# Kernel tuning notes

Measured on AMD Instinct MI355X. Metric: run time of the kernel, lower is better.

The kernel has to match this reference:

```python
import jax, jax.numpy as jnp
import numpy as np

NUM_HEADS = 4
WINDOW_SIZE = 7
DILATION = 1


def local_mask(height, width, window_size, dilation):
    """[N, N] bool mask: True where token i may attend to token j (dilated 2D window)."""
    radius = window_size // 2
    rows = jnp.arange(height)
    cols = jnp.arange(width)
    r = jnp.repeat(rows, width)          # [N] row index of each flattened token
    c = jnp.tile(cols, height)           # [N] col index of each flattened token
    dr = r[:, None] - r[None, :]         # [N, N]
    dc = c[:, None] - c[None, :]
    within = (jnp.abs(dr) <= radius * dilation) & (jnpp_abs(dc) <= radius * dilation) if False else (
        (jnp.abs(dr) <= radius * dilation) & (jnp.abs(dc) <= radius * dilation)
    )
    on_grid = (dr % dilation == 0) & (dc % dilation == 0)
    return within & on_grid


def setup_inputs() -> dict:
    key = jax.random.key(0)
    kq, kk, kv = jax.random.split(key, 3)
    shape = (2, 64, 64, 64)  # (B, C, H, W)
    q = jax.random.normal(kq, shape, dtype=jnp.float32)
    k = jax.random.normal(kk, shape, dtype=jnp.float32)
    v = jax.random.normal(kv, shape, dtype=jnp.float32)
    return {"q": q, "k": k, "v": v}


def reference(q, k, v):
    B, C, H, W = q.shape
    nh = NUM_HEADS
    hd = C // nh
    N = H * W

    def to_seq(x):
        # (B, C, H, W) -> (B, nh, N, hd)
        x = x.reshape(B, nh, hd, H, W)
        return x.transpose(0, 1, 3, 4, 2).reshape(B, nh, N, hd)

    q_seq = to_seq(q)
    k_seq = to_seq(k)
    v_seq = to_seq(v)

    scale = 1.0 / jnp.sqrt(jnp.asarray(hd, dtype=q.dtype))
    scores = jnp.einsum("bhqd,bhkd->bhqk", q_seq, k_seq) * scale  # [B, nh, N, N]

    mask = local_mask(H, W, WINDOW_SIZE, DILATION)  # [N, N] bool
    neg = jnp.finfo(scores.dtype).min
    scores = jnp.where(mask[None, None, :, :], scores, neg)

    attn = jax.nn.softmax(scores, axis=-1)
    out = jnp.einsum("bhqk,bhkd->bhqd", attn, v_seq)  # [B, nh, N, hd]

    # (B, nh, N, hd) -> (B, C, H, W)
    out = out.reshape(B, nh, H, W, hd).transpose(0, 1, 4, 2, 3).reshape(B, C, H, W)
    return out
```

## Files before the change

### kernel.cpp

```cpp
#include <hip/hip_runtime.h>
#include <hip/hip_bf16.h>
#include <math.h>

#define HD  16
#define HW  4096
#define RAD 3

__device__ __forceinline__ float dpp_shl1(float x) {
#if defined(__has_builtin) && __has_builtin(__builtin_amdgcn_update_dpp)
    return __int_as_float(__builtin_amdgcn_update_dpp(
        0, __float_as_int(x), 0x130 , 0xf, 0xf, true));
#else
    int l = (int)(threadIdx.x & 63);
    return __shfl(x, l + 1, 64);
#endif
}
__device__ __forceinline__ float dpp_shr1(float x) {
#if defined(__has_builtin) && __has_builtin(__builtin_amdgcn_update_dpp)
    return __int_as_float(__builtin_amdgcn_update_dpp(
        0, __float_as_int(x), 0x138 , 0xf, 0xf, true));
#else
    int l = (int)(threadIdx.x & 63);
    return __shfl(x, l - 1, 64);
#endif
}

__global__ __launch_bounds__(512, 2)
void local_attn_kernel(const float* __restrict__ q,
                       const float* __restrict__ k,
                       const float* __restrict__ v,
                       float* __restrict__ out) {
    __shared__ __align__(16) float mb[512 * 34];

    const int tid = threadIdx.x;
    const int c   = tid & 63;
    const int w   = tid >> 6;

    const int bid = blockIdx.x;
    const int r0  = (bid & 31) * 2;
    const int h   = (bid >> 5) & 3;
    const int b   = bid >> 7;
    const int base = (b * 4 + h) * (HD * HW);

    const int  rr     = r0 - RAD + w;
    const bool rvalid = ((unsigned)rr < 64u);
    const bool do0    = rvalid && (w <= 6);
    const bool do1    = rvalid && (w >= 1);
    const int  rrc    = rr < 0 ? 0 : (rr > 63 ? 63 : rr);

    const int pos0 = r0 * 64 + c;
    float kd[HD], vd[HD], qv0[HD], qv1[HD];
#pragma unroll
    for (int d = 0; d < HD; ++d) {
        kd[d]  = k[base + d * HW + rrc * 64 + c];
        vd[d]  = v[base + d * HW + rrc * 64 + c];
        qv0[d] = q[base + d * HW + pos0] * 0.25f;
        qv1[d] = q[base + d * HW + pos0 + 64] * 0.25f;
    }

    float s0[7], s1[7];
#pragma unroll
    for (int j = 0; j < 7; ++j) { s0[j] = 0.0f; s1[j] = 0.0f; }

#pragma unroll
    for (int d = 0; d < HD; ++d) {
        float kc  = kd[d];
        float kp1 = dpp_shl1(kc), kp2 = dpp_shl1(kp1), kp3 = dpp_shl1(kp2);
        float km1 = dpp_shr1(kc), km2 = dpp_shr1(km1), km3 = dpp_shr1(km2);
        float a0 = qv0[d], a1 = qv1[d];
        s0[0] = fmaf(a0, km3, s0[0]);  s1[0] = fmaf(a1, km3, s1[0]);
        s0[1] = fmaf(a0, km2, s0[1]);  s1[1] = fmaf(a1, km2, s1[1]);
        s0[2] = fmaf(a0, km1, s0[2]);  s1[2] = fmaf(a1, km1, s1[2]);
        s0[3] = fmaf(a0, kc,  s0[3]);  s1[3] = fmaf(a1, kc,  s1[3]);
        s0[4] = fmaf(a0, kp1, s0[4]);  s1[4] = fmaf(a1, kp1, s1[4]);
        s0[5] = fmaf(a0, kp2, s0[5]);  s1[5] = fmaf(a1, kp2, s1[5]);
        s0[6] = fmaf(a0, kp3, s0[6]);  s1[6] = fmaf(a1, kp3, s1[6]);
    }

    float l0 = 0.0f, l1 = 0.0f;
#pragma unroll
    for (int j = 0; j < 7; ++j) {
        bool okc = ((unsigned)(c + j - RAD) < 64u);
        float p0 = (okc && do0) ? __expf(s0[j]) : 0.0f;
        float p1 = (okc && do1) ? __expf(s1[j]) : 0.0f;
        s0[j] = p0;  l0 += p0;
        s1[j] = p1;  l1 += p1;
    }

    float acc0[HD], acc1[HD];
#pragma unroll
    for (int d = 0; d < HD; ++d) {
        float vc  = vd[d];
        float vp1 = dpp_shl1(vc), vp2 = dpp_shl1(vp1), vp3 = dpp_shl1(vp2);
        float vm1 = dpp_shr1(vc), vm2 = dpp_shr1(vm1), vm3 = dpp_shr1(vm2);
        float a0, a1;
        a0 = s0[0] * vm3;            a1 = s1[0] * vm3;
        a0 = fmaf(s0[1], vm2, a0);   a1 = fmaf(s1[1], vm2, a1);
        a0 = fmaf(s0[2], vm1, a0);   a1 = fmaf(s1[2], vm1, a1);
        a0 = fmaf(s0[3], vc,  a0);   a1 = fmaf(s1[3], vc,  a1);
        a0 = fmaf(s0[4], vp1, a0);   a1 = fmaf(s1[4], vp1, a1);
        a0 = fmaf(s0[5], vp2, a0);   a1 = fmaf(s1[5], vp2, a1);
        a0 = fmaf(s0[6], vp3, a0);   a1 = fmaf(s1[6], vp3, a1);
        acc0[d] = a0;  acc1[d] = a1;
    }

    const int bs = (w * 64 + c) * 34;
#pragma unroll
    for (int d = 0; d < HD; d += 2) {
        *(float2*)&mb[bs + d]      = make_float2(acc0[d], acc0[d + 1]);
        *(float2*)&mb[bs + 16 + d] = make_float2(acc1[d], acc1[d + 1]);
    }
    *(float2*)&mb[bs + 32] = make_float2(l0, l1);
    __syncthreads();

    const int qq = w >> 2;
    const int dq = (w & 3) * 4;

    float lt = 0.0f;
#pragma unroll
    for (int s = 0; s < 8; ++s)
        lt += mb[(s * 64 + c) * 34 + 32 + qq];
    const float invl = 1.0f / lt;

    float a[4] = {0.0f, 0.0f, 0.0f, 0.0f};
#pragma unroll
    for (int s = 0; s < 8; ++s) {
        const int rb = (s * 64 + c) * 34 + qq * 16 + dq;
        float2 x0 = *(const float2*)&mb[rb];
        float2 x1 = *(const float2*)&mb[rb + 2];
        a[0] += x0.x;  a[1] += x0.y;  a[2] += x1.x;  a[3] += x1.y;
    }
#pragma unroll
    for (int i = 0; i < 4; ++i)
        out[base + (dq + i) * HW + (r0 + qq) * 64 + c] = a[i] * invl;
}

extern "C" void kernel_launch(void* const* d_in, const int* in_sizes, int n_in,
                              void* d_out, int out_size, void* d_ws, size_t ws_size,
                              hipStream_t stream) {
    const float* q = (const float*)d_in[0];
    const float* k = (const float*)d_in[1];
    const float* v = (const float*)d_in[2];
    float* out = (float*)d_out;

    int queries = out_size / HD;
    int blocks  = queries / 128;
    local_attn_kernel<<<blocks, 512, 0, stream>>>(q, k, v, out);
}
```

Before: 10.23 us.

## Stage K/V via async global-to-LDS loads and share Q through LDS

K and V tiles are now brought into shared memory with 16-byte global_load_lds transfers distributed across all waves, instead of each thread issuing 16 scalar strided loads per tensor. Q is loaded once per block into LDS (each element read once rather than by all 8 waves redundantly), then read per-d during the score loop. The shared buffer is reused for the reduction stage after an extra barrier. This cuts redundant global Q traffic and widens load granularity, at the cost of extra barriers and LDS reads in the inner loops.

```diff
diff --git a/kernel.cpp b/kernel.cpp
--- a/kernel.cpp
+++ b/kernel.cpp
@@ -30,7 +30,10 @@
                        const float* __restrict__ k,
                        const float* __restrict__ v,
                        float* __restrict__ out) {
-    __shared__ __align__(16) float mb[512 * 34];
+    __shared__ float lds[18944];
+    float* ldsK = lds;
+    float* ldsV = lds + 8192;
+    float* ldsQ = lds + 16384;
 
     const int tid = threadIdx.x;
     const int c   = tid & 63;
@@ -42,21 +45,44 @@
     const int b   = bid >> 7;
     const int base = (b * 4 + h) * (HD * HW);
 
+#pragma unroll
+    for (int ii = 0; ii < 8; ++ii) {
+        int ci = w * 8 + ii;
+        int cj = ci & 31;
+        const float* src = (ci < 32) ? (k + base) : (v + base);
+        float* dst = (ci < 32) ? ldsK : ldsV;
+        int s  = cj * 4 + (c >> 4);
+        int d  = s >> 3;
+        int hr = s & 7;
+        int rr = r0 - RAD + hr;
+        rr = rr < 0 ? 0 : (rr > 63 ? 63 : rr);
+        const float* g = src + d * HW + rr * 64 + (c & 15) * 4;
+#if defined(__has_builtin) && __has_builtin(__builtin_amdgcn_global_load_lds)
+        __builtin_amdgcn_global_load_lds(
+            (const __attribute__((address_space(1))) void*)g,
+            (__attribute__((address_space(3))) void*)&dst[cj * 256], 16, 0, 0);
+#else
+        *(float4*)&dst[cj * 256 + c * 4] = *(const float4*)g;
+#endif
+    }
+
+    {
+        const int rq = w >> 2;
+        const int dg = (w & 3) * 4;
+        const int prow = (r0 + rq) * 64 + c;
+#pragma unroll
+        for (int i = 0; i < 4; ++i) {
+            float x = q[base + (dg + i) * HW + prow] * 0.25f;
+            ldsQ[(dg + i) * 128 + rq * 64 + c] = x;
+        }
+    }
+    __syncthreads();
+
     const int  rr     = r0 - RAD + w;
     const bool rvalid = ((unsigned)rr < 64u);
     const bool do0    = rvalid && (w <= 6);
     const bool do1    = rvalid && (w >= 1);
-    const int  rrc    = rr < 0 ? 0 : (rr > 63 ? 63 : rr);
-
-    const int pos0 = r0 * 64 + c;
-    float kd[HD], vd[HD], qv0[HD], qv1[HD];
-#pragma unroll
-    for (int d = 0; d < HD; ++d) {
-        kd[d]  = k[base + d * HW + rrc * 64 + c];
-        vd[d]  = v[base + d * HW + rrc * 64 + c];
-        qv0[d] = q[base + d * HW + pos0] * 0.25f;
-        qv1[d] = q[base + d * HW + pos0 + 64] * 0.25f;
-    }
+    const int  lrow   = w * 64 + c;
 
     float s0[7], s1[7];
 #pragma unroll
@@ -64,10 +90,11 @@
 
 #pragma unroll
     for (int d = 0; d < HD; ++d) {
-        float kc  = kd[d];
+        float kc  = ldsK[d * 512 + lrow];
+        float a0  = ldsQ[d * 128 + c];
+        float a1  = ldsQ[d * 128 + 64 + c];
         float kp1 = dpp_shl1(kc), kp2 = dpp_shl1(kp1), kp3 = dpp_shl1(kp2);
         float km1 = dpp_shr1(kc), km2 = dpp_shr1(km1), km3 = dpp_shr1(km2);
-        float a0 = qv0[d], a1 = qv1[d];
         s0[0] = fmaf(a0, km3, s0[0]);  s1[0] = fmaf(a1, km3, s1[0]);
         s0[1] = fmaf(a0, km2, s0[1]);  s1[1] = fmaf(a1, km2, s1[1]);
         s0[2] = fmaf(a0, km1, s0[2]);  s1[2] = fmaf(a1, km1, s1[2]);
@@ -90,7 +117,7 @@
     float acc0[HD], acc1[HD];
 #pragma unroll
     for (int d = 0; d < HD; ++d) {
-        float vc  = vd[d];
+        float vc  = ldsV[d * 512 + lrow];
         float vp1 = dpp_shl1(vc), vp2 = dpp_shl1(vp1), vp3 = dpp_shl1(vp2);
         float vm1 = dpp_shr1(vc), vm2 = dpp_shr1(vm1), vm3 = dpp_shr1(vm2);
         float a0, a1;
@@ -104,13 +131,15 @@
         acc0[d] = a0;  acc1[d] = a1;
     }
 
-    const int bs = (w * 64 + c) * 34;
+    __syncthreads();
+
+    const int bs = tid * 34;
 #pragma unroll
     for (int d = 0; d < HD; d += 2) {
-        *(float2*)&mb[bs + d]      = make_float2(acc0[d], acc0[d + 1]);
-        *(float2*)&mb[bs + 16 + d] = make_float2(acc1[d], acc1[d + 1]);
+        *(float2*)&lds[bs + d]      = make_float2(acc0[d], acc0[d + 1]);
+        *(float2*)&lds[bs + 16 + d] = make_float2(acc1[d], acc1[d + 1]);
     }
-    *(float2*)&mb[bs + 32] = make_float2(l0, l1);
+    *(float2*)&lds[bs + 32] = make_float2(l0, l1);
     __syncthreads();
 
     const int qq = w >> 2;
@@ -119,15 +148,15 @@
     float lt = 0.0f;
 #pragma unroll
     for (int s = 0; s < 8; ++s)
-        lt += mb[(s * 64 + c) * 34 + 32 + qq];
+        lt += lds[(s * 64 + c) * 34 + 32 + qq];
     const float invl = 1.0f / lt;
 
     float a[4] = {0.0f, 0.0f, 0.0f, 0.0f};
 #pragma unroll
     for (int s = 0; s < 8; ++s) {
         const int rb = (s * 64 + c) * 34 + qq * 16 + dq;
-        float2 x0 = *(const float2*)&mb[rb];
-        float2 x1 = *(const float2*)&mb[rb + 2];
+        float2 x0 = *(const float2*)&lds[rb];
+        float2 x1 = *(const float2*)&lds[rb + 2];
         a[0] += x0.x;  a[1] += x0.y;  a[2] += x1.x;  a[3] += x1.y;
     }
 #pragma unroll
```

After: 10.44 us. +2.1%, slower.
